# Kernel optimization log

Hardware: AMD Instinct MI355X
Metric: run time of the kernel (lower is better)

## Reference

```python
import jax, jax.numpy as jnp
import numpy as np

NUM_NODES = 4096
IN_DIM = 16
HIDDEN = 64
OUT_DIM = 32
HEADS = 4
NEG_SLOPE = 0.2
NEG_INF = -1e9


def _glorot(key, shape):
    fan_in, fan_out = shape[0], shape[-1]
    lim = jnp.sqrt(6.0 / (fan_in + fan_out))
    return jax.random.uniform(key, shape, jnp.float32, -lim, lim)


def setup_inputs() -> dict:
    key = jax.random.key(0)
    ks = jax.random.split(key, 8)
    B = 2
    return {
        "x": jax.random.normal(ks[0], (B, NUM_NODES, IN_DIM), jnp.float32),
        "embedding": _glorot(ks[1], (NUM_NODES, HIDDEN)),
        "W_proj": _glorot(ks[2], (IN_DIM, HIDDEN)),
        "b_proj": jnp.zeros((HIDDEN,), jnp.float32),
        "W1": _glorot(ks[3], (HIDDEN, HIDDEN)),  # heads=4, 16 per head, concat -> 64
        "att1_src": _glorot(ks[4], (HEADS, HIDDEN // HEADS)),
        "att1_dst": _glorot(ks[5], (HEADS, HIDDEN // HEADS)),
        "b1": jnp.zeros((HIDDEN,), jnp.float32),
        "W2": _glorot(ks[6], (HIDDEN, OUT_DIM)),  # heads=4, 8 per head, concat -> 32
        "att2_src": _glorot(ks[7], (HEADS, OUT_DIM // HEADS)),
        "att2_dst": _glorot(jax.random.fold_in(key, 99), (HEADS, OUT_DIM // HEADS)),
        "b2": jnp.zeros((OUT_DIM,), jnp.float32),
    }


def _gat(x, mask, W, a_src, a_dst, b):
    """Dense masked GAT layer. x: [B,N,Fin], mask: [N,N] bool (shared over batch).

    Equivalent to GATConv over edge list tf.where(adj > 0.5): for each target i,
    softmax over neighbors j of LeakyReLU(a_dst.Wh_i + a_src.Wh_j), aggregate Wh_j.
    """
    B, N, _ = x.shape
    H, F = a_src.shape
    h = (x @ W).reshape(B, N, H, F)                       # [B,N,H,F]
    s_src = jnp.einsum('bnhf,hf->bnh', h, a_src)          # per-source score
    s_dst = jnp.einsum('bnhf,hf->bnh', h, a_dst)          # per-target score
    e = s_dst[:, :, None, :] + s_src[:, None, :, :]       # [B,i,j,H]
    e = jnp.where(e > 0, e, NEG_SLOPE * e)                # LeakyReLU(0.2)
    e = jnp.where(mask[None, :, :, None], e, NEG_INF)
    alpha = jax.nn.softmax(e, axis=2)                     # softmax over neighbors j
    out = jnp.einsum('bijh,bjhf->bihf', alpha, h).reshape(B, N, H * F)
    return out + b


def reference(x, embedding, W_proj, b_proj, W1, att1_src, att1_dst, b1,
              W2, att2_src, att2_dst, b2):
    # AdaptiveAdjacency: cosine similarity of l2-normalized node embeddings
    ne = embedding / jnp.linalg.norm(embedding, axis=-1, keepdims=True)
    adj = ne @ ne.T                                       # [N,N], same for all batch
    mask = adj > 0.5                                      # edge set (incl. self-loops)

    h = x @ W_proj + b_proj                               # Dense proj -> hidden
    h = jax.nn.relu(_gat(h, mask, W1, att1_src, att1_dst, b1))
    return _gat(h, mask, W2, att2_src, att2_dst, b2)
```

## Files before the change

### kernel.cpp

```cpp
#include <hip/hip_runtime.h>
#include <hip/hip_bf16.h>
#include <stdint.h>

#define N_NODES 4096
#define BATCH 2

typedef __attribute__((ext_vector_type(8))) short short8v;
typedef __attribute__((ext_vector_type(4))) unsigned short ushort4v;
typedef __attribute__((ext_vector_type(4))) float f32x4;

#define GLL16(gsrc, ldst) \
    __builtin_amdgcn_global_load_lds((const __attribute__((address_space(1))) void*)(gsrc), \
                                     (__attribute__((address_space(3))) void*)(ldst), 16, 0, 0)

static __device__ inline unsigned short f2bf_rn(float x) {
    unsigned u = __float_as_uint(x);
    unsigned r = (u + 0x7FFFu + ((u >> 16) & 1u)) >> 16;
    return (unsigned short)r;
}
static __device__ inline float bf2f(unsigned short b) {
    return __uint_as_float(((unsigned)b) << 16);
}
static __device__ inline float rl(float v, int k) {
    return __uint_as_float(__builtin_amdgcn_readlane(__float_as_uint(v), k));
}

__global__ __launch_bounds__(256) void k1_kernel(
        const float* __restrict__ emb,
        unsigned short* __restrict__ ne_hi, unsigned short* __restrict__ ne_lo,
        const float* __restrict__ x, const float* __restrict__ Wp,
        const float* __restrict__ bp, const float* __restrict__ W1,
        const float* __restrict__ a1s, const float* __restrict__ a1d,
        float* __restrict__ h1out, float* __restrict__ ssrc, float* __restrict__ sdst) {
    int t = threadIdx.x;
    if (blockIdx.x < 256) {
        int row = blockIdx.x * 16 + (t >> 4);
        int l16 = t & 15;
        float4 v = *(const float4*)&emb[(size_t)row * 64 + l16 * 4];
        float s = v.x * v.x + v.y * v.y + v.z * v.z + v.w * v.w;
#pragma unroll
        for (int m = 8; m >= 1; m >>= 1) s += __shfl_xor(s, m);
        float inv = 1.f / sqrtf(s);
        float n0 = v.x * inv, n1 = v.y * inv, n2 = v.z * inv, n3 = v.w * inv;
        ushort4v h = {f2bf_rn(n0), f2bf_rn(n1), f2bf_rn(n2), f2bf_rn(n3)};
        ushort4v lo = {f2bf_rn(n0 - bf2f(h.x)), f2bf_rn(n1 - bf2f(h.y)),
                       f2bf_rn(n2 - bf2f(h.z)), f2bf_rn(n3 - bf2f(h.w))};
        *(ushort4v*)&ne_hi[(size_t)row * 64 + l16 * 4] = h;
        *(ushort4v*)&ne_lo[(size_t)row * 64 + l16 * 4] = lo;
    } else {
        int b = blockIdx.x - 256;
        int w = t >> 6, l = t & 63;
        int row0 = b * 32 + w * 8;

        float xv[8];
#pragma unroll
        for (int r = 0; r < 8; ++r) xv[r] = x[(size_t)(row0 + r) * 16 + (l & 15)];

        float h0[8];
        float bpv = bp[l];
#pragma unroll
        for (int r = 0; r < 8; ++r) h0[r] = bpv;
#pragma unroll
        for (int k = 0; k < 16; ++k) {
            float wk = Wp[k * 64 + l];
#pragma unroll
            for (int r = 0; r < 8; ++r) h0[r] += rl(xv[r], k) * wk;
        }

        float h1[8] = {0.f, 0.f, 0.f, 0.f, 0.f, 0.f, 0.f, 0.f};
#pragma unroll
        for (int k = 0; k < 64; ++k) {
            float wk = W1[k * 64 + l];
#pragma unroll
            for (int r = 0; r < 8; ++r) h1[r] += rl(h0[r], k) * wk;
        }

        float as_ = a1s[l], ad_ = a1d[l];
#pragma unroll
        for (int r = 0; r < 8; ++r) {
            h1out[(size_t)(row0 + r) * 64 + l] = h1[r];
            float ps = h1[r] * as_, pd = h1[r] * ad_;
#pragma unroll
            for (int m = 8; m >= 1; m >>= 1) {
                ps += __shfl_xor(ps, m);
                pd += __shfl_xor(pd, m);
            }
            if ((l & 15) == 0) {
                ssrc[(size_t)(row0 + r) * 4 + (l >> 4)] = ps;
                sdst[(size_t)(row0 + r) * 4 + (l >> 4)] = pd;
            }
        }
    }
}

__global__ __launch_bounds__(256) void adj_mfma_kernel(
        const unsigned short* __restrict__ hi, const unsigned short* __restrict__ lo,
        unsigned long long* __restrict__ mask) {
    __shared__ unsigned short Ah[128 * 64];
    __shared__ unsigned short Al[128 * 64];
    __shared__ unsigned short Bh[128 * 64];
    __shared__ unsigned short Bl[128 * 64];
    int t = threadIdx.x;
    int w = t >> 6, l = t & 63;
    int i0 = blockIdx.y * 128, j0 = blockIdx.x * 128;

    int cr = l >> 3;
    int slot = (l & 7) ^ cr;
#pragma unroll
    for (int q = 0; q < 4; ++q) {
        int lr = w * 32 + q * 8;
        size_t ga = (size_t)(i0 + lr + cr) * 64 + slot * 8;
        size_t gb = (size_t)(j0 + lr + cr) * 64 + slot * 8;
        GLL16(hi + ga, &Ah[lr * 64]);
        GLL16(lo + ga, &Al[lr * 64]);
        GLL16(hi + gb, &Bh[lr * 64]);
        GLL16(lo + gb, &Bl[lr * 64]);
    }
    __syncthreads();

    int fr = l & 15;
    int s0 = l >> 4;
    int r7 = l & 7;
    short8v aH[2][2], aL[2][2];
#pragma unroll
    for (int rt = 0; rt < 2; ++rt) {
        int base = (w * 32 + rt * 16 + fr) * 64;
        aH[rt][0] = *(const short8v*)&Ah[base + ((s0 ^ r7) << 3)];
        aH[rt][1] = *(const short8v*)&Ah[base + (((s0 + 4) ^ r7) << 3)];
        aL[rt][0] = *(const short8v*)&Al[base + ((s0 ^ r7) << 3)];
        aL[rt][1] = *(const short8v*)&Al[base + (((s0 + 4) ^ r7) << 3)];
    }

    f32x4 acc[2][8];
#pragma unroll
    for (int rt = 0; rt < 2; ++rt)
#pragma unroll
        for (int js = 0; js < 8; ++js) acc[rt][js] = (f32x4){0.f, 0.f, 0.f, 0.f};

#pragma unroll
    for (int js = 0; js < 8; ++js) {
        int bbase = (js * 16 + fr) * 64;
        short8v bH0 = *(const short8v*)&Bh[bbase + ((s0 ^ r7) << 3)];
        short8v bH1 = *(const short8v*)&Bh[bbase + (((s0 + 4) ^ r7) << 3)];
        short8v bL0 = *(const short8v*)&Bl[bbase + ((s0 ^ r7) << 3)];
        short8v bL1 = *(const short8v*)&Bl[bbase + (((s0 + 4) ^ r7) << 3)];
#pragma unroll
        for (int rt = 0; rt < 2; ++rt) {
            f32x4 a = acc[rt][js];
            a = __builtin_amdgcn_mfma_f32_16x16x32_bf16(aH[rt][0], bH0, a, 0, 0, 0);
            a = __builtin_amdgcn_mfma_f32_16x16x32_bf16(aH[rt][1], bH1, a, 0, 0, 0);
            a = __builtin_amdgcn_mfma_f32_16x16x32_bf16(aH[rt][0], bL0, a, 0, 0, 0);
            a = __builtin_amdgcn_mfma_f32_16x16x32_bf16(aH[rt][1], bL1, a, 0, 0, 0);
            a = __builtin_amdgcn_mfma_f32_16x16x32_bf16(aL[rt][0], bH0, a, 0, 0, 0);
            a = __builtin_amdgcn_mfma_f32_16x16x32_bf16(aL[rt][1], bH1, a, 0, 0, 0);
            acc[rt][js] = a;
        }
    }

    int shift = ((l & 15) >> 2) * 16;
    int r = l & 3;
#pragma unroll
    for (int rt = 0; rt < 2; ++rt) {
#pragma unroll
        for (int ws_ = 0; ws_ < 2; ++ws_) {
            unsigned long long w64 = 0;
#pragma unroll
            for (int js2 = 0; js2 < 4; ++js2) {
                f32x4 a = acc[rt][ws_ * 4 + js2];
                unsigned long long c0 = __ballot(a[0] > 0.5f);
                unsigned long long c1 = __ballot(a[1] > 0.5f);
                unsigned long long c2 = __ballot(a[2] > 0.5f);
                unsigned long long c3 = __ballot(a[3] > 0.5f);
                unsigned long long sel = r == 0 ? c0 : r == 1 ? c1 : r == 2 ? c2 : c3;
                w64 |= ((sel >> shift) & 0xFFFFULL) << (js2 * 16);
            }
            if (l < 16)
                mask[(size_t)(i0 + w * 32 + rt * 16 + l) * 64 + blockIdx.x * 2 + ws_] = w64;
        }
    }
}

__global__ __launch_bounds__(256) void agg1_fused_kernel(
        const float* __restrict__ h1, const float* __restrict__ ssrc,
        const float* __restrict__ sdst, const unsigned long long* __restrict__ mask,
        const float* __restrict__ b1, const float* __restrict__ W2,
        const float* __restrict__ a2s, const float* __restrict__ a2d,
        float* __restrict__ h2out, float* __restrict__ s2s, float* __restrict__ s2d) {
    int row = blockIdx.x * 4 + (threadIdx.x >> 6);
    int i = row & (N_NODES - 1);
    int bN = row - i;
    int t = threadIdx.x & 63;
    int hh = t >> 4;

    float sd = sdst[(size_t)row * 4 + hh];
    unsigned long long myword = mask[(size_t)i * 64 + t];

    float m = -1e30f, denom = 0.f, acc = 0.f;
    unsigned long long nz = __ballot(myword != 0ULL);
    while (nz) {
        int lw = __ffsll(nz) - 1;
        nz &= nz - 1;
        unsigned long long wbits = __shfl(myword, lw);
        while (wbits) {
            int bpos = __ffsll(wbits) - 1;
            wbits &= wbits - 1;
            int j = (lw << 6) + bpos;
            float e = sd + ssrc[(size_t)(bN + j) * 4 + hh];
            e = e > 0.f ? e : 0.2f * e;
            float mn = fmaxf(m, e);
            float cf = __expf(m - mn);
            float wg = __expf(e - mn);
            float hv = h1[(size_t)(bN + j) * 64 + t];
            denom = denom * cf + wg;
            acc = acc * cf + wg * hv;
            m = mn;
        }
    }
    float o = fmaxf(acc / denom + b1[t], 0.f);

    int l2 = t & 31;
    float acc2 = 0.f;
#pragma unroll
    for (int k = 0; k < 64; ++k) acc2 += rl(o, k) * W2[k * 32 + l2];

    float ps = acc2 * a2s[l2], pd = acc2 * a2d[l2];
#pragma unroll
    for (int mm = 4; mm >= 1; mm >>= 1) {
        ps += __shfl_xor(ps, mm);
        pd += __shfl_xor(pd, mm);
    }
    if (t < 32) {
        h2out[(size_t)row * 32 + t] = acc2;
        if ((t & 7) == 0) {
            s2s[(size_t)row * 4 + (t >> 3)] = ps;
            s2d[(size_t)row * 4 + (t >> 3)] = pd;
        }
    }
}

__global__ __launch_bounds__(256) void agg2_kernel(
        const float* __restrict__ hfeat, const float* __restrict__ ssrc,
        const float* __restrict__ sdst, const unsigned long long* __restrict__ mask,
        const float* __restrict__ bias, float* __restrict__ out) {
    int row = blockIdx.x * 4 + (threadIdx.x >> 6);
    int i = row & (N_NODES - 1);
    int bN = row - i;
    int t = threadIdx.x & 63;
    int tt = t & 31;
    int hh = tt >> 3;

    float sd = sdst[(size_t)row * 4 + hh];
    unsigned long long myword = mask[(size_t)i * 64 + t];

    float m = -1e30f, denom = 0.f, acc = 0.f;
    unsigned long long nz = __ballot(myword != 0ULL);
    while (nz) {
        int lw = __ffsll(nz) - 1;
        nz &= nz - 1;
        unsigned long long wbits = __shfl(myword, lw);
        while (wbits) {
            int bpos = __ffsll(wbits) - 1;
            wbits &= wbits - 1;
            int j = (lw << 6) + bpos;
            float e = sd + ssrc[(size_t)(bN + j) * 4 + hh];
            e = e > 0.f ? e : 0.2f * e;
            float mn = fmaxf(m, e);
            float cf = __expf(m - mn);
            float wg = __expf(e - mn);
            float hv = hfeat[(size_t)(bN + j) * 32 + tt];
            denom = denom * cf + wg;
            acc = acc * cf + wg * hv;
            m = mn;
        }
    }
    float o = acc / denom + bias[tt];
    if (t < 32) out[(size_t)row * 32 + tt] = o;
}

extern "C" void kernel_launch(void* const* d_in, const int* in_sizes, int n_in,
                              void* d_out, int out_size, void* d_ws, size_t ws_size,
                              hipStream_t stream) {
    const float* x   = (const float*)d_in[0];
    const float* emb = (const float*)d_in[1];
    const float* Wp  = (const float*)d_in[2];
    const float* bp  = (const float*)d_in[3];
    const float* W1  = (const float*)d_in[4];
    const float* a1s = (const float*)d_in[5];
    const float* a1d = (const float*)d_in[6];
    const float* b1  = (const float*)d_in[7];
    const float* W2  = (const float*)d_in[8];
    const float* a2s = (const float*)d_in[9];
    const float* a2d = (const float*)d_in[10];
    const float* b2  = (const float*)d_in[11];

    const int ROWS = BATCH * N_NODES;

    char* w = (char*)d_ws;
    unsigned short* ne_hi = (unsigned short*)w;  w += (size_t)N_NODES * 64 * 2;
    unsigned short* ne_lo = (unsigned short*)w;  w += (size_t)N_NODES * 64 * 2;
    unsigned long long* mask = (unsigned long long*)w; w += (size_t)N_NODES * 64 * 8;
    float* h1  = (float*)w;                      w += (size_t)ROWS * 64 * 4;
    float* s1s = (float*)w;                      w += (size_t)ROWS * 4 * 4;
    float* s1d = (float*)w;                      w += (size_t)ROWS * 4 * 4;
    float* h2  = (float*)w;                      w += (size_t)ROWS * 32 * 4;
    float* s2s = (float*)w;                      w += (size_t)ROWS * 4 * 4;
    float* s2d = (float*)w;                      w += (size_t)ROWS * 4 * 4;

    k1_kernel<<<dim3(512), dim3(256), 0, stream>>>(
        emb, ne_hi, ne_lo, x, Wp, bp, W1, a1s, a1d, h1, s1s, s1d);
    adj_mfma_kernel<<<dim3(32, 32), dim3(256), 0, stream>>>(ne_hi, ne_lo, mask);
    agg1_fused_kernel<<<dim3(ROWS / 4), dim3(256), 0, stream>>>(
        h1, s1s, s1d, mask, b1, W2, a2s, a2d, h2, s2s, s2d);
    agg2_kernel<<<dim3(ROWS / 4), dim3(256), 0, stream>>>(
        h2, s2s, s2d, mask, b2, (float*)d_out);
}
```

Before: 37.43 us.

## Fuse four launches into one persistent kernel with software grid barriers

Replaces the four separate kernel launches (embedding normalize/projection, adjacency MFMA, layer-1 aggregation, layer-2 aggregation) with a single persistent kernel of 256 blocks. The blocks loop over the old work units and synchronise between stages with atomic-counter grid barriers, reset by a memset before launch. The aim is to remove per-launch overhead and the gaps between kernels. In exchange, each stage runs on fewer concurrent blocks, the aggregation stages lose latency hiding, and the barriers only work if all 256 blocks are resident at once.

```diff
diff --git a/kernel.cpp b/kernel.cpp
--- a/kernel.cpp
+++ b/kernel.cpp
@@ -4,6 +4,7 @@
 
 #define N_NODES 4096
 #define BATCH 2
+#define GRID 256
 
 typedef __attribute__((ext_vector_type(8))) short short8v;
 typedef __attribute__((ext_vector_type(4))) unsigned short ushort4v;
@@ -25,274 +26,303 @@
     return __uint_as_float(__builtin_amdgcn_readlane(__float_as_uint(v), k));
 }
 
-__global__ __launch_bounds__(256) void k1_kernel(
-        const float* __restrict__ emb,
-        unsigned short* __restrict__ ne_hi, unsigned short* __restrict__ ne_lo,
-        const float* __restrict__ x, const float* __restrict__ Wp,
-        const float* __restrict__ bp, const float* __restrict__ W1,
-        const float* __restrict__ a1s, const float* __restrict__ a1d,
-        float* __restrict__ h1out, float* __restrict__ ssrc, float* __restrict__ sdst) {
-    int t = threadIdx.x;
-    if (blockIdx.x < 256) {
-        int row = blockIdx.x * 16 + (t >> 4);
-        int l16 = t & 15;
-        float4 v = *(const float4*)&emb[(size_t)row * 64 + l16 * 4];
-        float s = v.x * v.x + v.y * v.y + v.z * v.z + v.w * v.w;
-#pragma unroll
-        for (int m = 8; m >= 1; m >>= 1) s += __shfl_xor(s, m);
-        float inv = 1.f / sqrtf(s);
-        float n0 = v.x * inv, n1 = v.y * inv, n2 = v.z * inv, n3 = v.w * inv;
-        ushort4v h = {f2bf_rn(n0), f2bf_rn(n1), f2bf_rn(n2), f2bf_rn(n3)};
-        ushort4v lo = {f2bf_rn(n0 - bf2f(h.x)), f2bf_rn(n1 - bf2f(h.y)),
-                       f2bf_rn(n2 - bf2f(h.z)), f2bf_rn(n3 - bf2f(h.w))};
-        *(ushort4v*)&ne_hi[(size_t)row * 64 + l16 * 4] = h;
-        *(ushort4v*)&ne_lo[(size_t)row * 64 + l16 * 4] = lo;
-    } else {
-        int b = blockIdx.x - 256;
-        int w = t >> 6, l = t & 63;
-        int row0 = b * 32 + w * 8;
-
-        float xv[8];
-#pragma unroll
-        for (int r = 0; r < 8; ++r) xv[r] = x[(size_t)(row0 + r) * 16 + (l & 15)];
-
-        float h0[8];
-        float bpv = bp[l];
-#pragma unroll
-        for (int r = 0; r < 8; ++r) h0[r] = bpv;
-#pragma unroll
-        for (int k = 0; k < 16; ++k) {
-            float wk = Wp[k * 64 + l];
-#pragma unroll
-            for (int r = 0; r < 8; ++r) h0[r] += rl(xv[r], k) * wk;
-        }
-
-        float h1[8] = {0.f, 0.f, 0.f, 0.f, 0.f, 0.f, 0.f, 0.f};
-#pragma unroll
-        for (int k = 0; k < 64; ++k) {
-            float wk = W1[k * 64 + l];
-#pragma unroll
-            for (int r = 0; r < 8; ++r) h1[r] += rl(h0[r], k) * wk;
-        }
-
-        float as_ = a1s[l], ad_ = a1d[l];
-#pragma unroll
-        for (int r = 0; r < 8; ++r) {
-            h1out[(size_t)(row0 + r) * 64 + l] = h1[r];
-            float ps = h1[r] * as_, pd = h1[r] * ad_;
-#pragma unroll
-            for (int m = 8; m >= 1; m >>= 1) {
-                ps += __shfl_xor(ps, m);
-                pd += __shfl_xor(pd, m);
-            }
-            if ((l & 15) == 0) {
-                ssrc[(size_t)(row0 + r) * 4 + (l >> 4)] = ps;
-                sdst[(size_t)(row0 + r) * 4 + (l >> 4)] = pd;
-            }
-        }
-    }
-}
-
-__global__ __launch_bounds__(256) void adj_mfma_kernel(
-        const unsigned short* __restrict__ hi, const unsigned short* __restrict__ lo,
-        unsigned long long* __restrict__ mask) {
+struct KParams {
+    const float* emb;
+    const float* x;
+    const float* Wp;
+    const float* bp;
+    const float* W1;
+    const float* a1s;
+    const float* a1d;
+    const float* b1;
+    const float* W2;
+    const float* a2s;
+    const float* a2d;
+    const float* b2;
+    unsigned short* ne_hi;
+    unsigned short* ne_lo;
+    unsigned long long* mask;
+    float* h1;
+    float* s1s;
+    float* s1d;
+    float* h2;
+    float* s2s;
+    float* s2d;
+    float* out;
+    unsigned* bar;
+};
+
+static __device__ inline void grid_bar(unsigned* ctr) {
+    __syncthreads();
+    if (threadIdx.x == 0) {
+        __threadfence();
+        atomicAdd(ctr, 1u);
+        while (__hip_atomic_load(ctr, __ATOMIC_ACQUIRE,
+                                 __HIP_MEMORY_SCOPE_AGENT) < (unsigned)GRID)
+            __builtin_amdgcn_s_sleep(2);
+    }
+    __syncthreads();
+}
+
+__global__ __launch_bounds__(256) void fused_kernel(KParams p) {
     __shared__ unsigned short Ah[128 * 64];
     __shared__ unsigned short Al[128 * 64];
     __shared__ unsigned short Bh[128 * 64];
     __shared__ unsigned short Bl[128 * 64];
+
     int t = threadIdx.x;
+    int bid = blockIdx.x;
     int w = t >> 6, l = t & 63;
-    int i0 = blockIdx.y * 128, j0 = blockIdx.x * 128;
-
-    int cr = l >> 3;
-    int slot = (l & 7) ^ cr;
-#pragma unroll
-    for (int q = 0; q < 4; ++q) {
-        int lr = w * 32 + q * 8;
-        size_t ga = (size_t)(i0 + lr + cr) * 64 + slot * 8;
-        size_t gb = (size_t)(j0 + lr + cr) * 64 + slot * 8;
-        GLL16(hi + ga, &Ah[lr * 64]);
-        GLL16(lo + ga, &Al[lr * 64]);
-        GLL16(hi + gb, &Bh[lr * 64]);
-        GLL16(lo + gb, &Bl[lr * 64]);
-    }
-    __syncthreads();
-
-    int fr = l & 15;
-    int s0 = l >> 4;
-    int r7 = l & 7;
-    short8v aH[2][2], aL[2][2];
-#pragma unroll
-    for (int rt = 0; rt < 2; ++rt) {
-        int base = (w * 32 + rt * 16 + fr) * 64;
-        aH[rt][0] = *(const short8v*)&Ah[base + ((s0 ^ r7) << 3)];
-        aH[rt][1] = *(const short8v*)&Ah[base + (((s0 + 4) ^ r7) << 3)];
-        aL[rt][0] = *(const short8v*)&Al[base + ((s0 ^ r7) << 3)];
-        aL[rt][1] = *(const short8v*)&Al[base + (((s0 + 4) ^ r7) << 3)];
-    }
-
-    f32x4 acc[2][8];
-#pragma unroll
-    for (int rt = 0; rt < 2; ++rt)
-#pragma unroll
-        for (int js = 0; js < 8; ++js) acc[rt][js] = (f32x4){0.f, 0.f, 0.f, 0.f};
-
-#pragma unroll
-    for (int js = 0; js < 8; ++js) {
-        int bbase = (js * 16 + fr) * 64;
-        short8v bH0 = *(const short8v*)&Bh[bbase + ((s0 ^ r7) << 3)];
-        short8v bH1 = *(const short8v*)&Bh[bbase + (((s0 + 4) ^ r7) << 3)];
-        short8v bL0 = *(const short8v*)&Bl[bbase + ((s0 ^ r7) << 3)];
-        short8v bL1 = *(const short8v*)&Bl[bbase + (((s0 + 4) ^ r7) << 3)];
+
+#pragma unroll 1
+    for (int u = bid; u < 512; u += GRID) {
+        if (u < 256) {
+            int row = u * 16 + (t >> 4);
+            int l16 = t & 15;
+            float4 v = *(const float4*)&p.emb[(size_t)row * 64 + l16 * 4];
+            float s = v.x * v.x + v.y * v.y + v.z * v.z + v.w * v.w;
+#pragma unroll
+            for (int m = 8; m >= 1; m >>= 1) s += __shfl_xor(s, m);
+            float inv = 1.f / sqrtf(s);
+            float n0 = v.x * inv, n1 = v.y * inv, n2 = v.z * inv, n3 = v.w * inv;
+            ushort4v h = {f2bf_rn(n0), f2bf_rn(n1), f2bf_rn(n2), f2bf_rn(n3)};
+            ushort4v lo = {f2bf_rn(n0 - bf2f(h.x)), f2bf_rn(n1 - bf2f(h.y)),
+                           f2bf_rn(n2 - bf2f(h.z)), f2bf_rn(n3 - bf2f(h.w))};
+            *(ushort4v*)&p.ne_hi[(size_t)row * 64 + l16 * 4] = h;
+            *(ushort4v*)&p.ne_lo[(size_t)row * 64 + l16 * 4] = lo;
+        } else {
+            int row0 = (u - 256) * 32 + w * 8;
+
+            float xv[8];
+#pragma unroll
+            for (int r = 0; r < 8; ++r)
+                xv[r] = p.x[(size_t)(row0 + r) * 16 + (l & 15)];
+
+            float h0[8];
+            float bpv = p.bp[l];
+#pragma unroll
+            for (int r = 0; r < 8; ++r) h0[r] = bpv;
+#pragma unroll
+            for (int k = 0; k < 16; ++k) {
+                float wk = p.Wp[k * 64 + l];
+#pragma unroll
+                for (int r = 0; r < 8; ++r) h0[r] += rl(xv[r], k) * wk;
+            }
+
+            float h1v[8] = {0.f, 0.f, 0.f, 0.f, 0.f, 0.f, 0.f, 0.f};
+#pragma unroll
+            for (int k = 0; k < 64; ++k) {
+                float wk = p.W1[k * 64 + l];
+#pragma unroll
+                for (int r = 0; r < 8; ++r) h1v[r] += rl(h0[r], k) * wk;
+            }
+
+            float as_ = p.a1s[l], ad_ = p.a1d[l];
+#pragma unroll
+            for (int r = 0; r < 8; ++r) {
+                p.h1[(size_t)(row0 + r) * 64 + l] = h1v[r];
+                float ps = h1v[r] * as_, pd = h1v[r] * ad_;
+#pragma unroll
+                for (int m = 8; m >= 1; m >>= 1) {
+                    ps += __shfl_xor(ps, m);
+                    pd += __shfl_xor(pd, m);
+                }
+                if ((l & 15) == 0) {
+                    p.s1s[(size_t)(row0 + r) * 4 + (l >> 4)] = ps;
+                    p.s1d[(size_t)(row0 + r) * 4 + (l >> 4)] = pd;
+                }
+            }
+        }
+    }
+    grid_bar(p.bar + 0);
+
+#pragma unroll 1
+    for (int tile = bid; tile < 1024; tile += GRID) {
+        int bi = tile >> 5, bj = tile & 31;
+        int i0 = bi * 128, j0 = bj * 128;
+
+        int cr = l >> 3;
+        int slot = (l & 7) ^ cr;
+#pragma unroll
+        for (int q = 0; q < 4; ++q) {
+            int lr = w * 32 + q * 8;
+            size_t ga = (size_t)(i0 + lr + cr) * 64 + slot * 8;
+            size_t gb = (size_t)(j0 + lr + cr) * 64 + slot * 8;
+            GLL16(p.ne_hi + ga, &Ah[lr * 64]);
+            GLL16(p.ne_lo + ga, &Al[lr * 64]);
+            GLL16(p.ne_hi + gb, &Bh[lr * 64]);
+            GLL16(p.ne_lo + gb, &Bl[lr * 64]);
+        }
+        __syncthreads();
+
+        int fr = l & 15;
+        int s0 = l >> 4;
+        int r7 = l & 7;
+        short8v aH[2][2], aL[2][2];
 #pragma unroll
         for (int rt = 0; rt < 2; ++rt) {
-            f32x4 a = acc[rt][js];
-            a = __builtin_amdgcn_mfma_f32_16x16x32_bf16(aH[rt][0], bH0, a, 0, 0, 0);
-            a = __builtin_amdgcn_mfma_f32_16x16x32_bf16(aH[rt][1], bH1, a, 0, 0, 0);
-            a = __builtin_amdgcn_mfma_f32_16x16x32_bf16(aH[rt][0], bL0, a, 0, 0, 0);
-            a = __builtin_amdgcn_mfma_f32_16x16x32_bf16(aH[rt][1], bL1, a, 0, 0, 0);
-            a = __builtin_amdgcn_mfma_f32_16x16x32_bf16(aL[rt][0], bH0, a, 0, 0, 0);
-            a = __builtin_amdgcn_mfma_f32_16x16x32_bf16(aL[rt][1], bH1, a, 0, 0, 0);
-            acc[rt][js] = a;
-        }
-    }
-
-    int shift = ((l & 15) >> 2) * 16;
-    int r = l & 3;
-#pragma unroll
-    for (int rt = 0; rt < 2; ++rt) {
-#pragma unroll
-        for (int ws_ = 0; ws_ < 2; ++ws_) {
-            unsigned long long w64 = 0;
-#pragma unroll
-            for (int js2 = 0; js2 < 4; ++js2) {
-                f32x4 a = acc[rt][ws_ * 4 + js2];
-                unsigned long long c0 = __ballot(a[0] > 0.5f);
-                unsigned long long c1 = __ballot(a[1] > 0.5f);
-                unsigned long long c2 = __ballot(a[2] > 0.5f);
-                unsigned long long c3 = __ballot(a[3] > 0.5f);
-                unsigned long long sel = r == 0 ? c0 : r == 1 ? c1 : r == 2 ? c2 : c3;
-                w64 |= ((sel >> shift) & 0xFFFFULL) << (js2 * 16);
-            }
-            if (l < 16)
-                mask[(size_t)(i0 + w * 32 + rt * 16 + l) * 64 + blockIdx.x * 2 + ws_] = w64;
-        }
-    }
-}
-
-__global__ __launch_bounds__(256) void agg1_fused_kernel(
-        const float* __restrict__ h1, const float* __restrict__ ssrc,
-        const float* __restrict__ sdst, const unsigned long long* __restrict__ mask,
-        const float* __restrict__ b1, const float* __restrict__ W2,
-        const float* __restrict__ a2s, const float* __restrict__ a2d,
-        float* __restrict__ h2out, float* __restrict__ s2s, float* __restrict__ s2d) {
-    int row = blockIdx.x * 4 + (threadIdx.x >> 6);
-    int i = row & (N_NODES - 1);
-    int bN = row - i;
-    int t = threadIdx.x & 63;
-    int hh = t >> 4;
-
-    float sd = sdst[(size_t)row * 4 + hh];
-    unsigned long long myword = mask[(size_t)i * 64 + t];
-
-    float m = -1e30f, denom = 0.f, acc = 0.f;
-    unsigned long long nz = __ballot(myword != 0ULL);
-    while (nz) {
-        int lw = __ffsll(nz) - 1;
-        nz &= nz - 1;
-        unsigned long long wbits = __shfl(myword, lw);
-        while (wbits) {
-            int bpos = __ffsll(wbits) - 1;
-            wbits &= wbits - 1;
-            int j = (lw << 6) + bpos;
-            float e = sd + ssrc[(size_t)(bN + j) * 4 + hh];
-            e = e > 0.f ? e : 0.2f * e;
-            float mn = fmaxf(m, e);
-            float cf = __expf(m - mn);
-            float wg = __expf(e - mn);
-            float hv = h1[(size_t)(bN + j) * 64 + t];
-            denom = denom * cf + wg;
-            acc = acc * cf + wg * hv;
-            m = mn;
-        }
-    }
-    float o = fmaxf(acc / denom + b1[t], 0.f);
-
-    int l2 = t & 31;
-    float acc2 = 0.f;
-#pragma unroll
-    for (int k = 0; k < 64; ++k) acc2 += rl(o, k) * W2[k * 32 + l2];
-
-    float ps = acc2 * a2s[l2], pd = acc2 * a2d[l2];
-#pragma unroll
-    for (int mm = 4; mm >= 1; mm >>= 1) {
-        ps += __shfl_xor(ps, mm);
-        pd += __shfl_xor(pd, mm);
-    }
-    if (t < 32) {
-        h2out[(size_t)row * 32 + t] = acc2;
-        if ((t & 7) == 0) {
-            s2s[(size_t)row * 4 + (t >> 3)] = ps;
-            s2d[(size_t)row * 4 + (t >> 3)] = pd;
-        }
-    }
-}
-
-__global__ __launch_bounds__(256) void agg2_kernel(
-        const float* __restrict__ hfeat, const float* __restrict__ ssrc,
-        const float* __restrict__ sdst, const unsigned long long* __restrict__ mask,
-        const float* __restrict__ bias, float* __restrict__ out) {
-    int row = blockIdx.x * 4 + (threadIdx.x >> 6);
-    int i = row & (N_NODES - 1);
-    int bN = row - i;
-    int t = threadIdx.x & 63;
-    int tt = t & 31;
-    int hh = tt >> 3;
-
-    float sd = sdst[(size_t)row * 4 + hh];
-    unsigned long long myword = mask[(size_t)i * 64 + t];
-
-    float m = -1e30f, denom = 0.f, acc = 0.f;
-    unsigned long long nz = __ballot(myword != 0ULL);
-    while (nz) {
-        int lw = __ffsll(nz) - 1;
-        nz &= nz - 1;
-        unsigned long long wbits = __shfl(myword, lw);
-        while (wbits) {
-            int bpos = __ffsll(wbits) - 1;
-            wbits &= wbits - 1;
-            int j = (lw << 6) + bpos;
-            float e = sd + ssrc[(size_t)(bN + j) * 4 + hh];
-            e = e > 0.f ? e : 0.2f * e;
-            float mn = fmaxf(m, e);
-            float cf = __expf(m - mn);
-            float wg = __expf(e - mn);
-            float hv = hfeat[(size_t)(bN + j) * 32 + tt];
-            denom = denom * cf + wg;
-            acc = acc * cf + wg * hv;
-            m = mn;
-        }
-    }
-    float o = acc / denom + bias[tt];
-    if (t < 32) out[(size_t)row * 32 + tt] = o;
+            int base = (w * 32 + rt * 16 + fr) * 64;
+            aH[rt][0] = *(const short8v*)&Ah[base + ((s0 ^ r7) << 3)];
+            aH[rt][1] = *(const short8v*)&Ah[base + (((s0 + 4) ^ r7) << 3)];
+            aL[rt][0] = *(const short8v*)&Al[base + ((s0 ^ r7) << 3)];
+            aL[rt][1] = *(const short8v*)&Al[base + (((s0 + 4) ^ r7) << 3)];
+        }
+
+        f32x4 acc[2][8];
+#pragma unroll
+        for (int rt = 0; rt < 2; ++rt)
+#pragma unroll
+            for (int js = 0; js < 8; ++js) acc[rt][js] = (f32x4){0.f, 0.f, 0.f, 0.f};
+
+#pragma unroll
+        for (int js = 0; js < 8; ++js) {
+            int bbase = (js * 16 + fr) * 64;
+            short8v bH0 = *(const short8v*)&Bh[bbase + ((s0 ^ r7) << 3)];
+            short8v bH1 = *(const short8v*)&Bh[bbase + (((s0 + 4) ^ r7) << 3)];
+            short8v bL0 = *(const short8v*)&Bl[bbase + ((s0 ^ r7) << 3)];
+            short8v bL1 = *(const short8v*)&Bl[bbase + (((s0 + 4) ^ r7) << 3)];
+#pragma unroll
+            for (int rt = 0; rt < 2; ++rt) {
+                f32x4 a = acc[rt][js];
+                a = __builtin_amdgcn_mfma_f32_16x16x32_bf16(aH[rt][0], bH0, a, 0, 0, 0);
+                a = __builtin_amdgcn_mfma_f32_16x16x32_bf16(aH[rt][1], bH1, a, 0, 0, 0);
+                a = __builtin_amdgcn_mfma_f32_16x16x32_bf16(aH[rt][0], bL0, a, 0, 0, 0);
+                a = __builtin_amdgcn_mfma_f32_16x16x32_bf16(aH[rt][1], bL1, a, 0, 0, 0);
+                a = __builtin_amdgcn_mfma_f32_16x16x32_bf16(aL[rt][0], bH0, a, 0, 0, 0);
+                a = __builtin_amdgcn_mfma_f32_16x16x32_bf16(aL[rt][1], bH1, a, 0, 0, 0);
+                acc[rt][js] = a;
+            }
+        }
+
+        int shift = ((l & 15) >> 2) * 16;
+        int r = l & 3;
+#pragma unroll
+        for (int rt = 0; rt < 2; ++rt) {
+#pragma unroll
+            for (int ws_ = 0; ws_ < 2; ++ws_) {
+                unsigned long long w64 = 0;
+#pragma unroll
+                for (int js2 = 0; js2 < 4; ++js2) {
+                    f32x4 a = acc[rt][ws_ * 4 + js2];
+                    unsigned long long c0 = __ballot(a[0] > 0.5f);
+                    unsigned long long c1 = __ballot(a[1] > 0.5f);
+                    unsigned long long c2 = __ballot(a[2] > 0.5f);
+                    unsigned long long c3 = __ballot(a[3] > 0.5f);
+                    unsigned long long sel = r == 0 ? c0 : r == 1 ? c1 : r == 2 ? c2 : c3;
+                    w64 |= ((sel >> shift) & 0xFFFFULL) << (js2 * 16);
+                }
+                if (l < 16)
+                    p.mask[(size_t)(i0 + w * 32 + rt * 16 + l) * 64 + bj * 2 + ws_] = w64;
+            }
+        }
+        __syncthreads();
+    }
+    grid_bar(p.bar + 1);
+
+    {
+        int hh1 = l >> 4;
+        int l2 = l & 31;
+#pragma unroll 1
+        for (int u = bid; u < 512; u += GRID) {
+#pragma unroll 1
+            for (int rr = 0; rr < 4; ++rr) {
+                int row = u * 16 + w * 4 + rr;
+                int i = row & (N_NODES - 1);
+                int bN = row - i;
+
+                float sd = p.s1d[(size_t)row * 4 + hh1];
+                unsigned long long myword = p.mask[(size_t)i * 64 + l];
+
+                float m = -1e30f, denom = 0.f, acc = 0.f;
+                unsigned long long nz = __ballot(myword != 0ULL);
+                while (nz) {
+                    int lw = __ffsll(nz) - 1;
+                    nz &= nz - 1;
+                    unsigned long long wbits = __shfl(myword, lw);
+                    while (wbits) {
+                        int bpos = __ffsll(wbits) - 1;
+                        wbits &= wbits - 1;
+                        int j = (lw << 6) + bpos;
+                        float e = sd + p.s1s[(size_t)(bN + j) * 4 + hh1];
+                        e = e > 0.f ? e : 0.2f * e;
+                        float mn = fmaxf(m, e);
+                        float cf = __expf(m - mn);
+                        float wg = __expf(e - mn);
+                        float hv = p.h1[(size_t)(bN + j) * 64 + l];
+                        denom = denom * cf + wg;
+                        acc = acc * cf + wg * hv;
+                        m = mn;
+                    }
+                }
+                float o = fmaxf(acc / denom + p.b1[l], 0.f);
+
+                float acc2 = 0.f;
+#pragma unroll
+                for (int k = 0; k < 64; ++k) acc2 += rl(o, k) * p.W2[k * 32 + l2];
+
+                float ps = acc2 * p.a2s[l2], pd = acc2 * p.a2d[l2];
+#pragma unroll
+                for (int mm = 4; mm >= 1; mm >>= 1) {
+                    ps += __shfl_xor(ps, mm);
+                    pd += __shfl_xor(pd, mm);
+                }
+                if (l < 32) {
+                    p.h2[(size_t)row * 32 + l] = acc2;
+                    if ((l & 7) == 0) {
+                        p.s2s[(size_t)row * 4 + (l >> 3)] = ps;
+                        p.s2d[(size_t)row * 4 + (l >> 3)] = pd;
+                    }
+                }
+            }
+        }
+    }
+    grid_bar(p.bar + 2);
+
+    {
+        int tt = l & 31;
+        int hh2 = tt >> 3;
+#pragma unroll 1
+        for (int u = bid; u < 512; u += GRID) {
+#pragma unroll 1
+            for (int rr = 0; rr < 4; ++rr) {
+                int row = u * 16 + w * 4 + rr;
+                int i = row & (N_NODES - 1);
+                int bN = row - i;
+
+                float sd = p.s2d[(size_t)row * 4 + hh2];
+                unsigned long long myword = p.mask[(size_t)i * 64 + l];
+
+                float m = -1e30f, denom = 0.f, acc = 0.f;
+                unsigned long long nz = __ballot(myword != 0ULL);
+                while (nz) {
+                    int lw = __ffsll(nz) - 1;
+                    nz &= nz - 1;
+                    unsigned long long wbits = __shfl(myword, lw);
+                    while (wbits) {
+                        int bpos = __ffsll(wbits) - 1;
+                        wbits &= wbits - 1;
+                        int j = (lw << 6) + bpos;
+                        float e = sd + p.s2s[(size_t)(bN + j) * 4 + hh2];
+                        e = e > 0.f ? e : 0.2f * e;
+                        float mn = fmaxf(m, e);
+                        float cf = __expf(m - mn);
+                        float wg = __expf(e - mn);
+                        float hv = p.h2[(size_t)(bN + j) * 32 + tt];
+                        denom = denom * cf + wg;
+                        acc = acc * cf + wg * hv;
+                        m = mn;
+                    }
+                }
+                float o = acc / denom + p.b2[tt];
+                if (l < 32) p.out[(size_t)row * 32 + tt] = o;
+            }
+        }
+    }
 }
 
 extern "C" void kernel_launch(void* const* d_in, const int* in_sizes, int n_in,
                               void* d_out, int out_size, void* d_ws, size_t ws_size,
                               hipStream_t stream) {
-    const float* x   = (const float*)d_in[0];
-    const float* emb = (const float*)d_in[1];
-    const float* Wp  = (const float*)d_in[2];
-    const float* bp  = (const float*)d_in[3];
-    const float* W1  = (const float*)d_in[4];
-    const float* a1s = (const float*)d_in[5];
-    const float* a1d = (const float*)d_in[6];
-    const float* b1  = (const float*)d_in[7];
-    const float* W2  = (const float*)d_in[8];
-    const float* a2s = (const float*)d_in[9];
-    const float* a2d = (const float*)d_in[10];
-    const float* b2  = (const float*)d_in[11];
-
     const int ROWS = BATCH * N_NODES;
 
     char* w = (char*)d_ws;
@@ -305,12 +335,33 @@
     float* h2  = (float*)w;                      w += (size_t)ROWS * 32 * 4;
     float* s2s = (float*)w;                      w += (size_t)ROWS * 4 * 4;
     float* s2d = (float*)w;                      w += (size_t)ROWS * 4 * 4;
-
-    k1_kernel<<<dim3(512), dim3(256), 0, stream>>>(
-        emb, ne_hi, ne_lo, x, Wp, bp, W1, a1s, a1d, h1, s1s, s1d);
-    adj_mfma_kernel<<<dim3(32, 32), dim3(256), 0, stream>>>(ne_hi, ne_lo, mask);
-    agg1_fused_kernel<<<dim3(ROWS / 4), dim3(256), 0, stream>>>(
-        h1, s1s, s1d, mask, b1, W2, a2s, a2d, h2, s2s, s2d);
-    agg2_kernel<<<dim3(ROWS / 4), dim3(256), 0, stream>>>(
-        h2, s2s, s2d, mask, b2, (float*)d_out);
-}
+    unsigned* bar = (unsigned*)w;                w += 64;
+
+    KParams p;
+    p.emb = (const float*)d_in[1];
+    p.x   = (const float*)d_in[0];
+    p.Wp  = (const float*)d_in[2];
+    p.bp  = (const float*)d_in[3];
+    p.W1  = (const float*)d_in[4];
+    p.a1s = (const float*)d_in[5];
+    p.a1d = (const float*)d_in[6];
+    p.b1  = (const float*)d_in[7];
+    p.W2  = (const float*)d_in[8];
+    p.a2s = (const float*)d_in[9];
+    p.a2d = (const float*)d_in[10];
+    p.b2  = (const float*)d_in[11];
+    p.ne_hi = ne_hi;
+    p.ne_lo = ne_lo;
+    p.mask = mask;
+    p.h1 = h1;
+    p.s1s = s1s;
+    p.s1d = s1d;
+    p.h2 = h2;
+    p.s2s = s2s;
+    p.s2d = s2d;
+    p.out = (float*)d_out;
+    p.bar = bar;
+
+    hipMemsetAsync(bar, 0, 64, stream);
+    fused_kernel<<<dim3(GRID), dim3(256), 0, stream>>>(p);
+}
```

Result: slower. 106.8 us (+185.3%).

## Exploit adjacency symmetry in mask kernel and cache neighbor lists for layer 2

Applied to the files above, without the earlier changes.

The adjacency MFMA kernel now computes only the upper-triangular tile blocks and writes the mirrored tile by transposing the ballot bits through LDS, which roughly halves the matmul work. The first aggregation kernel also records up to 16 neighbor indices per node into a compact edge list. The second aggregation kernel iterates over that list instead of rescanning the 64-word bitmask, and falls back to the bitmask path for nodes with more neighbors. This trades some extra global writes and an LDS transpose for less matmul and mask-scan work, and relies on the cosine-similarity matrix being symmetric.

```diff
diff --git a/kernel.cpp b/kernel.cpp
--- a/kernel.cpp
+++ b/kernel.cpp
@@ -4,6 +4,7 @@
 
 #define N_NODES 4096
 #define BATCH 2
+#define EL_CAP 16
 
 typedef __attribute__((ext_vector_type(8))) short short8v;
 typedef __attribute__((ext_vector_type(4))) unsigned short ushort4v;
@@ -100,9 +101,11 @@
     __shared__ unsigned short Al[128 * 64];
     __shared__ unsigned short Bh[128 * 64];
     __shared__ unsigned short Bl[128 * 64];
+    int bi = blockIdx.y, bj = blockIdx.x;
+    if (bj < bi) return;
     int t = threadIdx.x;
     int w = t >> 6, l = t & 63;
-    int i0 = blockIdx.y * 128, j0 = blockIdx.x * 128;
+    int i0 = bi * 128, j0 = bj * 128;
 
     int cr = l >> 3;
     int slot = (l & 7) ^ cr;
@@ -157,25 +160,73 @@
         }
     }
 
-    int shift = ((l & 15) >> 2) * 16;
+    __syncthreads();
+    unsigned char* ldsT = (unsigned char*)Ah;
+    unsigned* ldsT32 = (unsigned*)Ah;
+
+    int c16 = l & 15;
+    int q = l >> 4;
+    int trt = q >> 1;
+    int rgb = (q & 1) * 2;
+    unsigned sh0 = c16 + 16 * rgb, sh1 = c16 + 16 * (rgb + 1);
+
+    int shift = (c16 >> 2) * 16;
     int r = l & 3;
 #pragma unroll
-    for (int rt = 0; rt < 2; ++rt) {
-#pragma unroll
-        for (int ws_ = 0; ws_ < 2; ++ws_) {
-            unsigned long long w64 = 0;
-#pragma unroll
-            for (int js2 = 0; js2 < 4; ++js2) {
-                f32x4 a = acc[rt][ws_ * 4 + js2];
-                unsigned long long c0 = __ballot(a[0] > 0.5f);
-                unsigned long long c1 = __ballot(a[1] > 0.5f);
-                unsigned long long c2 = __ballot(a[2] > 0.5f);
-                unsigned long long c3 = __ballot(a[3] > 0.5f);
-                unsigned long long sel = r == 0 ? c0 : r == 1 ? c1 : r == 2 ? c2 : c3;
-                w64 |= ((sel >> shift) & 0xFFFFULL) << (js2 * 16);
-            }
-            if (l < 16)
-                mask[(size_t)(i0 + w * 32 + rt * 16 + l) * 64 + blockIdx.x * 2 + ws_] = w64;
+    for (int ws_ = 0; ws_ < 2; ++ws_) {
+        unsigned long long w64_0 = 0, w64_1 = 0;
+#pragma unroll
+        for (int js2 = 0; js2 < 4; ++js2) {
+            int js = ws_ * 4 + js2;
+            f32x4 a0 = acc[0][js], a1 = acc[1][js];
+            unsigned long long B00 = __ballot(a0[0] > 0.5f);
+            unsigned long long B01 = __ballot(a0[1] > 0.5f);
+            unsigned long long B02 = __ballot(a0[2] > 0.5f);
+            unsigned long long B03 = __ballot(a0[3] > 0.5f);
+            unsigned long long B10 = __ballot(a1[0] > 0.5f);
+            unsigned long long B11 = __ballot(a1[1] > 0.5f);
+            unsigned long long B12 = __ballot(a1[2] > 0.5f);
+            unsigned long long B13 = __ballot(a1[3] > 0.5f);
+
+            unsigned long long sel0 = r == 0 ? B00 : r == 1 ? B01 : r == 2 ? B02 : B03;
+            unsigned long long sel1 = r == 0 ? B10 : r == 1 ? B11 : r == 2 ? B12 : B13;
+            w64_0 |= ((sel0 >> shift) & 0xFFFFULL) << (js2 * 16);
+            w64_1 |= ((sel1 >> shift) & 0xFFFFULL) << (js2 * 16);
+
+            if (bi != bj) {
+                unsigned long long s0_ = trt ? B10 : B00;
+                unsigned long long s1_ = trt ? B11 : B01;
+                unsigned long long s2_ = trt ? B12 : B02;
+                unsigned long long s3_ = trt ? B13 : B03;
+                unsigned p8 =
+                    ((unsigned)(s0_ >> sh0) & 1u) |
+                    (((unsigned)(s1_ >> sh0) & 1u) << 1) |
+                    (((unsigned)(s2_ >> sh0) & 1u) << 2) |
+                    (((unsigned)(s3_ >> sh0) & 1u) << 3) |
+                    (((unsigned)(s0_ >> sh1) & 1u) << 4) |
+                    (((unsigned)(s1_ >> sh1) & 1u) << 5) |
+                    (((unsigned)(s2_ >> sh1) & 1u) << 6) |
+                    (((unsigned)(s3_ >> sh1) & 1u) << 7);
+                ldsT[(js * 16 + c16) * 16 + w * 4 + q] = (unsigned char)p8;
+            }
+        }
+        if (l < 16) {
+            mask[(size_t)(i0 + w * 32 + 0 * 16 + l) * 64 + bj * 2 + ws_] = w64_0;
+            mask[(size_t)(i0 + w * 32 + 1 * 16 + l) * 64 + bj * 2 + ws_] = w64_1;
+        }
+    }
+
+    if (bi != bj) {
+        __syncthreads();
+        if (t < 128) {
+            unsigned u0 = ldsT32[t * 4 + 0];
+            unsigned u1 = ldsT32[t * 4 + 1];
+            unsigned u2 = ldsT32[t * 4 + 2];
+            unsigned u3 = ldsT32[t * 4 + 3];
+            unsigned long long word0 = (unsigned long long)u0 | ((unsigned long long)u1 << 32);
+            unsigned long long word1 = (unsigned long long)u2 | ((unsigned long long)u3 << 32);
+            mask[(size_t)(j0 + t) * 64 + bi * 2 + 0] = word0;
+            mask[(size_t)(j0 + t) * 64 + bi * 2 + 1] = word1;
         }
     }
 }
@@ -185,7 +236,8 @@
         const float* __restrict__ sdst, const unsigned long long* __restrict__ mask,
         const float* __restrict__ b1, const float* __restrict__ W2,
         const float* __restrict__ a2s, const float* __restrict__ a2d,
-        float* __restrict__ h2out, float* __restrict__ s2s, float* __restrict__ s2d) {
+        float* __restrict__ h2out, float* __restrict__ s2s, float* __restrict__ s2d,
+        int* __restrict__ ecnt, int* __restrict__ elist) {
     int row = blockIdx.x * 4 + (threadIdx.x >> 6);
     int i = row & (N_NODES - 1);
     int bN = row - i;
@@ -194,6 +246,8 @@
 
     float sd = sdst[(size_t)row * 4 + hh];
     unsigned long long myword = mask[(size_t)i * 64 + t];
+    bool emit = (row < N_NODES);
+    int cnt = 0;
 
     float m = -1e30f, denom = 0.f, acc = 0.f;
     unsigned long long nz = __ballot(myword != 0ULL);
@@ -205,6 +259,10 @@
             int bpos = __ffsll(wbits) - 1;
             wbits &= wbits - 1;
             int j = (lw << 6) + bpos;
+            if (emit) {
+                if (t == 0 && cnt < EL_CAP) elist[(size_t)i * EL_CAP + cnt] = j;
+                ++cnt;
+            }
             float e = sd + ssrc[(size_t)(bN + j) * 4 + hh];
             e = e > 0.f ? e : 0.2f * e;
             float mn = fmaxf(m, e);
@@ -216,6 +274,8 @@
             m = mn;
         }
     }
+    if (emit && t == 0) ecnt[i] = cnt;
+
     float o = fmaxf(acc / denom + b1[t], 0.f);
 
     int l2 = t & 31;
@@ -241,7 +301,8 @@
 __global__ __launch_bounds__(256) void agg2_kernel(
         const float* __restrict__ hfeat, const float* __restrict__ ssrc,
         const float* __restrict__ sdst, const unsigned long long* __restrict__ mask,
-        const float* __restrict__ bias, float* __restrict__ out) {
+        const float* __restrict__ bias, const int* __restrict__ ecnt,
+        const int* __restrict__ elist, float* __restrict__ out) {
     int row = blockIdx.x * 4 + (threadIdx.x >> 6);
     int i = row & (N_NODES - 1);
     int bN = row - i;
@@ -250,18 +311,13 @@
     int hh = tt >> 3;
 
     float sd = sdst[(size_t)row * 4 + hh];
-    unsigned long long myword = mask[(size_t)i * 64 + t];
+    int cnt = ecnt[i];
 
     float m = -1e30f, denom = 0.f, acc = 0.f;
-    unsigned long long nz = __ballot(myword != 0ULL);
-    while (nz) {
-        int lw = __ffsll(nz) - 1;
-        nz &= nz - 1;
-        unsigned long long wbits = __shfl(myword, lw);
-        while (wbits) {
-            int bpos = __ffsll(wbits) - 1;
-            wbits &= wbits - 1;
-            int j = (lw << 6) + bpos;
+    if (cnt <= EL_CAP) {
+#pragma unroll 1
+        for (int k = 0; k < cnt; ++k) {
+            int j = elist[(size_t)i * EL_CAP + k];
             float e = sd + ssrc[(size_t)(bN + j) * 4 + hh];
             e = e > 0.f ? e : 0.2f * e;
             float mn = fmaxf(m, e);
@@ -271,6 +327,28 @@
             denom = denom * cf + wg;
             acc = acc * cf + wg * hv;
             m = mn;
+        }
+    } else {
+        unsigned long long myword = mask[(size_t)i * 64 + t];
+        unsigned long long nz = __ballot(myword != 0ULL);
+        while (nz) {
+            int lw = __ffsll(nz) - 1;
+            nz &= nz - 1;
+            unsigned long long wbits = __shfl(myword, lw);
+            while (wbits) {
+                int bpos = __ffsll(wbits) - 1;
+                wbits &= wbits - 1;
+                int j = (lw << 6) + bpos;
+                float e = sd + ssrc[(size_t)(bN + j) * 4 + hh];
+                e = e > 0.f ? e : 0.2f * e;
+                float mn = fmaxf(m, e);
+                float cf = __expf(m - mn);
+                float wg = __expf(e - mn);
+                float hv = hfeat[(size_t)(bN + j) * 32 + tt];
+                denom = denom * cf + wg;
+                acc = acc * cf + wg * hv;
+                m = mn;
+            }
         }
     }
     float o = acc / denom + bias[tt];
@@ -305,12 +383,14 @@
     float* h2  = (float*)w;                      w += (size_t)ROWS * 32 * 4;
     float* s2s = (float*)w;                      w += (size_t)ROWS * 4 * 4;
     float* s2d = (float*)w;                      w += (size_t)ROWS * 4 * 4;
+    int* ecnt  = (int*)w;                        w += (size_t)N_NODES * 4;
+    int* elist = (int*)w;                        w += (size_t)N_NODES * EL_CAP * 4;
 
     k1_kernel<<<dim3(512), dim3(256), 0, stream>>>(
         emb, ne_hi, ne_lo, x, Wp, bp, W1, a1s, a1d, h1, s1s, s1d);
     adj_mfma_kernel<<<dim3(32, 32), dim3(256), 0, stream>>>(ne_hi, ne_lo, mask);
     agg1_fused_kernel<<<dim3(ROWS / 4), dim3(256), 0, stream>>>(
-        h1, s1s, s1d, mask, b1, W2, a2s, a2d, h2, s2s, s2d);
+        h1, s1s, s1d, mask, b1, W2, a2s, a2d, h2, s2s, s2d, ecnt, elist);
     agg2_kernel<<<dim3(ROWS / 4), dim3(256), 0, stream>>>(
-        h2, s2s, s2d, mask, b2, (float*)d_out);
-}
+        h2, s2s, s2d, mask, b2, ecnt, elist, (float*)d_out);
+}
```

Result: slower. 40.04 us (+7.0%).
